# Kernel optimization log

Hardware: AMD Instinct MI355X
Metric: run time of the kernel (lower is better)

Reference implementation:

```python
import jax, jax.numpy as jnp
import numpy as np

IMG_W, IMG_H = 128, 128
N_PTS = 256
MIN_D, MAX_D = 2.0, 6.0
FOCAL = 1.7320508  # 1/tan(fov/2), fov=60deg (FoVPerspectiveCameras default)
SCALING = 0.1      # scaling_factor default
EPS_EA = 1e-10     # pytorch3d EmissionAbsorptionRaymarcher eps


def setup_inputs() -> dict:
    key = jax.random.key(0)
    k1, k2 = jax.random.split(key)
    image3d = jax.random.uniform(k1, (1, 1, 128, 128, 128), jnp.float32)
    opacity = jax.random.uniform(k2, (1, 1, 128, 128, 128), jnp.float32)
    # row-vector camera convention (pytorch3d): p_cam = p_world @ R + T
    R = jnp.zeros((1, 3, 3), jnp.float32).at[:, jnp.arange(3), jnp.arange(3)].set(1.0)
    T = jnp.zeros((1, 3), jnp.float32).at[:, 2].set(4.0)
    return {"image3d": image3d, "opacity": opacity, "R": R, "T": T}


def _trilinear(vol, pts):
    """vol [C,D,H,W]; pts [N,3] xyz in [-1,1] (x->W, y->H, z->D).
    align_corners=True, zero padding outside. Returns [N,C]."""
    C, D, H, W = vol.shape
    x = (pts[:, 0] + 1.0) * 0.5 * (W - 1)
    y = (pts[:, 1] + 1.0) * 0.5 * (H - 1)
    z = (pts[:, 2] + 1.0) * 0.5 * (D - 1)
    x0 = jnp.floor(x); y0 = jnp.floor(y); z0 = jnp.floor(z)
    wx = x - x0; wy = y - y0; wz = z - z0
    vol_flat = vol.reshape(C, -1)
    out = jnp.zeros((pts.shape[0], C), vol.dtype)
    for dz in (0, 1):
        for dy in (0, 1):
            for dx in (0, 1):
                xi = (x0 + dx).astype(jnp.int32)
                yi = (y0 + dy).astype(jnp.int32)
                zi = (z0 + dz).astype(jnp.int32)
                valid = ((xi >= 0) & (xi < W) & (yi >= 0) & (yi < H)
                         & (zi >= 0) & (zi < D))
                w = ((wx if dx else 1.0 - wx) * (wy if dy else 1.0 - wy)
                     * (wz if dz else 1.0 - wz)) * valid.astype(vol.dtype)
                idx = ((jnp.clip(zi, 0, D - 1) * H + jnp.clip(yi, 0, H - 1)) * W
                       + jnp.clip(xi, 0, W - 1))
                vals = jnp.take(vol_flat, idx, axis=1)  # [C,N]
                out = out + w[:, None] * vals.T
    return out


def _forward(image3d, opacity, R, T):
    B = image3d.shape[0]
    features_vol = jnp.repeat(image3d, 3, axis=1)            # [B,3,D,H,W]
    densities_vol = opacity * SCALING                        # [B,1,D,H,W]
    Dv, Hv, Wv = image3d.shape[2:]
    shape = max(image3d.shape[1], image3d.shape[2])
    voxel = 3.0 / shape
    half_extent = voxel * (jnp.array([Wv, Hv, Dv], jnp.float32) - 1.0) / 2.0

    # NDC pixel grid (pytorch3d: +x left, +y up)
    xs = jnp.linspace(1.0, -1.0, IMG_W)
    ys = jnp.linspace(1.0, -1.0, IMG_H)
    gy, gx = jnp.meshgrid(ys, xs, indexing="ij")             # [H,W]
    dirs_cam = jnp.stack([gx / FOCAL, gy / FOCAL, jnp.ones_like(gx)], -1)  # [H,W,3]
    depths = jnp.linspace(MIN_D, MAX_D, N_PTS)               # [P]

    # row-vector transforms: p_world = (p_cam - T) @ R^T
    origins = jnp.einsum("bi,bji->bj", -T, R)                # camera centers [B,3]
    dirs_world = jnp.einsum("hwi,bji->bhwj", dirs_cam, R)    # [B,H,W,3]
    pts = (origins[:, None, None, None, :]
           + depths[None, None, None, :, None] * dirs_world[:, :, :, None, :])
    local = pts / half_extent                                # [B,H,W,P,3]

    pts_flat = local.reshape(B, -1, 3)
    feats = jax.vmap(_trilinear)(features_vol, pts_flat)
    feats = feats.reshape(B, IMG_H, IMG_W, N_PTS, 3)
    dens = jax.vmap(_trilinear)(densities_vol, pts_flat)
    dens = dens.reshape(B, IMG_H, IMG_W, N_PTS)

    # EmissionAbsorption raymarcher
    cum = jnp.cumprod((1.0 + EPS_EA) - dens, axis=-1)
    absorption = jnp.concatenate([jnp.ones_like(cum[..., :1]), cum[..., :-1]], -1)
    weights = dens * absorption
    feat_out = jnp.sum(weights[..., None] * feats, axis=-2)  # [B,H,W,3]
    opac = 1.0 - jnp.prod(1.0 - dens, axis=-1, keepdims=True)
    rgba = jnp.concatenate([feat_out, opac], axis=-1)        # [B,H,W,4]

    screen = jnp.transpose(rgba, (0, 3, 2, 1))               # permute(0,3,2,1)
    gray = screen[:, :3].mean(axis=1, keepdims=True)         # [B,1,W,H]
    st = (gray - gray.mean()) / (gray.std(ddof=1) + 1e-8)    # standardized
    out = (st - st.min() + 1e-8) / (st.max() - st.min() + 1e-8)  # normalized
    return out


def reference(image3d, opacity, R, T):
    return _forward(image3d, opacity, R, T)
```

## Files before the change

### kernel.cpp

```cpp
#include <hip/hip_runtime.h>
#include <math.h>


#define FOCAL 1.7320508f

__global__ __launch_bounds__(256) void render_kernel(
    const float* __restrict__ img, const float* __restrict__ opa,
    const float* __restrict__ Rm, const float* __restrict__ Tv,
    float2* __restrict__ partial, int nseg_shift)
{
  const int lane   = threadIdx.x & 63;
  const int waveid = threadIdx.x >> 6;
  const int wg     = (blockIdx.x << 2) + waveid;
  const int nseg   = 1 << nseg_shift;
  const int seg    = wg & (nseg - 1);
  const int pg     = wg >> nseg_shift;
  const int h      = pg >> 1;
  const int w      = ((pg & 1) << 6) | lane;

  const float R00=Rm[0], R01=Rm[1], R02=Rm[2];
  const float R10=Rm[3], R11=Rm[4], R12=Rm[5];
  const float R20=Rm[6], R21=Rm[7], R22=Rm[8];
  const float T0=Tv[0], T1=Tv[1], T2=Tv[2];

  const float ox = -(T0*R00 + T1*R01 + T2*R02);
  const float oy = -(T0*R10 + T1*R11 + T2*R12);
  const float oz = -(T0*R20 + T1*R21 + T2*R22);

  const float gx = 1.0f - (2.0f/127.0f) * (float)w;
  const float gy = 1.0f - (2.0f/127.0f) * (float)h;
  const float dcx = gx * (1.0f/FOCAL);
  const float dcy = gy * (1.0f/FOCAL);
  const float dwx = dcx*R00 + dcy*R01 + R02;
  const float dwy = dcx*R10 + dcy*R11 + R12;
  const float dwz = dcx*R20 + dcy*R21 + R22;

  const float s_he = (1.0f/1.48828125f) * 63.5f;
  const float ax = dwx * s_he, bx = ox * s_he + 63.5f;
  const float ay = dwy * s_he, by = oy * s_he + 63.5f;
  const float az = dwz * s_he, bz = oz * s_he + 63.5f;

  const int spseg = 256 >> nseg_shift;
  const int p0 = seg * spseg;

  float lp = 1.0f;
  float accl = 0.0f;

  for (int j = 0; j < spseg; ++j) {
    const float depth = 2.0f + (4.0f/255.0f) * (float)(p0 + j);
    const float x = bx + depth * ax;
    const float y = by + depth * ay;
    const float z = bz + depth * az;
    const float x0f = floorf(x), y0f = floorf(y), z0f = floorf(z);
    const float wx = x - x0f, wy = y - y0f, wz = z - z0f;
    const int x0 = (int)x0f, y0 = (int)y0f, z0 = (int)z0f;

    float feat = 0.0f, dens = 0.0f;
    if (x0 >= -1 && x0 <= 127 && y0 >= -1 && y0 <= 127 &&
        z0 >= -1 && z0 <= 127) {
      const float fx0 = (x0 >= 0)   ? (1.0f - wx) : 0.0f;
      const float fx1 = (x0 <= 126) ? wx          : 0.0f;
      const float fy0 = (y0 >= 0)   ? (1.0f - wy) : 0.0f;
      const float fy1 = (y0 <= 126) ? wy          : 0.0f;
      const float fz0 = (z0 >= 0)   ? (1.0f - wz) : 0.0f;
      const float fz1 = (z0 <= 126) ? wz          : 0.0f;
      const int ix0 = (x0 >= 0)   ? x0     : 0;
      const int ix1 = (x0 <= 126) ? x0 + 1 : 127;
      const int iy0 = ((y0 >= 0)   ? y0     : 0)   << 7;
      const int iy1 = ((y0 <= 126) ? y0 + 1 : 127) << 7;
      const int iz0 = ((z0 >= 0)   ? z0     : 0)   << 14;
      const int iz1 = ((z0 <= 126) ? z0 + 1 : 127) << 14;

      const int b00 = iz0 + iy0, b01 = iz0 + iy1;
      const int b10 = iz1 + iy0, b11 = iz1 + iy1;
      const float w00 = fz0*fy0, w01 = fz0*fy1, w10 = fz1*fy0, w11 = fz1*fy1;

      feat = w00*(fx0*img[b00+ix0] + fx1*img[b00+ix1])
           + w01*(fx0*img[b01+ix0] + fx1*img[b01+ix1])
           + w10*(fx0*img[b10+ix0] + fx1*img[b10+ix1])
           + w11*(fx0*img[b11+ix0] + fx1*img[b11+ix1]);
      dens = w00*(fx0*opa[b00+ix0] + fx1*opa[b00+ix1])
           + w01*(fx0*opa[b01+ix0] + fx1*opa[b01+ix1])
           + w10*(fx0*opa[b10+ix0] + fx1*opa[b10+ix1])
           + w11*(fx0*opa[b11+ix0] + fx1*opa[b11+ix1]);
    }
    const float d = dens * 0.1f;
    accl += feat * d * lp;
    lp   *= (1.0f - d);
  }

  partial[(seg << 14) + (h << 7) + w] = make_float2(accl, lp);
}

__global__ __launch_bounds__(256) void combine_kernel(
    const float2* __restrict__ partial, float* __restrict__ g,
    double* __restrict__ bstats, int nseg)
{
  const int tid = threadIdx.x;
  const int pid = (blockIdx.x << 8) + tid;

  float T = 1.0f, acc = 0.0f;
  for (int s = 0; s < nseg; ++s) {
    const float2 v = partial[(s << 14) + pid];
    acc += v.x * T;
    T *= v.y;
  }
  g[pid] = acc;

  double sum = (double)acc;
  double sq  = (double)acc * (double)acc;
  float mn = acc, mx = acc;
  #pragma unroll
  for (int off = 32; off >= 1; off >>= 1) {
    sum += __shfl_xor(sum, off, 64);
    sq  += __shfl_xor(sq,  off, 64);
    mn = fminf(mn, __shfl_xor(mn, off, 64));
    mx = fmaxf(mx, __shfl_xor(mx, off, 64));
  }
  __shared__ double s_sum[4], s_sq[4];
  __shared__ float  s_mn[4], s_mx[4];
  const int wv = tid >> 6;
  if ((tid & 63) == 0) { s_sum[wv]=sum; s_sq[wv]=sq; s_mn[wv]=mn; s_mx[wv]=mx; }
  __syncthreads();
  if (tid == 0) {
    double S = 0.0, Q = 0.0;
    float MN = s_mn[0], MX = s_mx[0];
    #pragma unroll
    for (int i = 0; i < 4; ++i) {
      S += s_sum[i]; Q += s_sq[i];
      MN = fminf(MN, s_mn[i]); MX = fmaxf(MX, s_mx[i]);
    }
    bstats[(blockIdx.x << 2) + 0] = S;
    bstats[(blockIdx.x << 2) + 1] = Q;
    bstats[(blockIdx.x << 2) + 2] = (double)MN;
    bstats[(blockIdx.x << 2) + 3] = (double)MX;
  }
}

__global__ __launch_bounds__(256) void finalize_kernel(
    const float* __restrict__ g, const double* __restrict__ bstats,
    float* __restrict__ out)
{
  __shared__ float sh[3];
  const int tid = threadIdx.x;
  if (tid < 64) {
    double S  = bstats[(tid << 2) + 0];
    double Q  = bstats[(tid << 2) + 1];
    double MN = bstats[(tid << 2) + 2];
    double MX = bstats[(tid << 2) + 3];
    #pragma unroll
    for (int off = 32; off >= 1; off >>= 1) {
      S += __shfl_xor(S, off, 64);
      Q += __shfl_xor(Q, off, 64);
      MN = fmin(MN, __shfl_xor(MN, off, 64));
      MX = fmax(MX, __shfl_xor(MX, off, 64));
    }
    if (tid == 0) {
      const double mean = S / 16384.0;
      double var = (Q - 16384.0 * mean * mean) / 16383.0;
      if (var < 0.0) var = 0.0;
      const float sdev = (float)sqrt(var) + 1e-8f;
      const float mnf = (float)MN, mxf = (float)MX;
      sh[0] = mnf;
      sh[1] = 1.0f / sdev;
      sh[2] = 1.0f / ((mxf - mnf) / sdev + 1e-8f);
    }
  }
  __syncthreads();
  const float mnv = sh[0], invs = sh[1], sc = sh[2];
  const int pid = (blockIdx.x << 8) + tid;
  const float v = g[pid];
  const int hh = pid >> 7, ww = pid & 127;
  out[(ww << 7) + hh] = ((v - mnv) * invs + 1e-8f) * sc;
}

extern "C" void kernel_launch(void* const* d_in, const int* in_sizes, int n_in,
                              void* d_out, int out_size, void* d_ws, size_t ws_size,
                              hipStream_t stream) {
  const float* img = (const float*)d_in[0];
  const float* opa = (const float*)d_in[1];
  const float* Rm  = (const float*)d_in[2];
  const float* Tv  = (const float*)d_in[3];
  float* out = (float*)d_out;

  int shift = 4;
  while (shift > 0) {
    const size_t need = ((size_t)131072 << shift) + 65536 + 2048;
    if (need <= ws_size) break;
    --shift;
  }
  const int nseg = 1 << shift;

  char* wsb = (char*)d_ws;
  float2* partial = (float2*)wsb;
  float*  g       = (float*)(wsb + ((size_t)131072 << shift));
  double* bstats  = (double*)(wsb + ((size_t)131072 << shift) + 65536);

  render_kernel<<<64 * nseg, 256, 0, stream>>>(img, opa, Rm, Tv, partial, shift);
  combine_kernel<<<64, 256, 0, stream>>>(partial, g, bstats, nseg);
  finalize_kernel<<<64, 256, 0, stream>>>(g, bstats, out);
}
```

Measured before the change: 98.67 us.

## Fuse render, segment combine and normalization into one kernel with last-block finalize

Merges the three launches into a single kernel. Each block handles 64 pixels with 8 waves, each wave marching one 32-sample segment, and the segments are combined through shared memory instead of a global partial buffer. Global statistics are reduced by whichever block finishes last, detected with an atomic counter, and that block writes the normalized output. This removes two launches and the partial-buffer round trip, but the ray march runs on 256 blocks instead of up to 1024, the final normalization pass is serialized onto one block, and a memset is added.

```diff
diff --git a/kernel.cpp b/kernel.cpp
--- a/kernel.cpp
+++ b/kernel.cpp
@@ -4,19 +4,18 @@
 
 #define FOCAL 1.7320508f
 
-__global__ __launch_bounds__(256) void render_kernel(
+__global__ __launch_bounds__(512) void dvr_kernel(
     const float* __restrict__ img, const float* __restrict__ opa,
     const float* __restrict__ Rm, const float* __restrict__ Tv,
-    float2* __restrict__ partial, int nseg_shift)
+    float* __restrict__ g, double* __restrict__ bstats,
+    unsigned int* __restrict__ counter, float* __restrict__ out)
 {
-  const int lane   = threadIdx.x & 63;
-  const int waveid = threadIdx.x >> 6;
-  const int wg     = (blockIdx.x << 2) + waveid;
-  const int nseg   = 1 << nseg_shift;
-  const int seg    = wg & (nseg - 1);
-  const int pg     = wg >> nseg_shift;
-  const int h      = pg >> 1;
-  const int w      = ((pg & 1) << 6) | lane;
+  const int tid  = threadIdx.x;
+  const int lane = tid & 63;
+  const int seg  = tid >> 6;
+  const int b    = blockIdx.x;
+  const int h    = b >> 1;
+  const int w    = ((b & 1) << 6) | lane;
 
   const float R00=Rm[0], R01=Rm[1], R02=Rm[2];
   const float R10=Rm[3], R11=Rm[4], R12=Rm[5];
@@ -36,21 +35,20 @@
   const float dwz = dcx*R20 + dcy*R21 + R22;
 
   const float s_he = (1.0f/1.48828125f) * 63.5f;
-  const float ax = dwx * s_he, bx = ox * s_he + 63.5f;
-  const float ay = dwy * s_he, by = oy * s_he + 63.5f;
-  const float az = dwz * s_he, bz = oz * s_he + 63.5f;
+  const float ax = dwx * s_he, bxc = ox * s_he + 63.5f;
+  const float ay = dwy * s_he, byc = oy * s_he + 63.5f;
+  const float az = dwz * s_he, bzc = oz * s_he + 63.5f;
 
-  const int spseg = 256 >> nseg_shift;
-  const int p0 = seg * spseg;
+  const int p0 = seg << 5;
 
   float lp = 1.0f;
   float accl = 0.0f;
 
-  for (int j = 0; j < spseg; ++j) {
+  for (int j = 0; j < 32; ++j) {
     const float depth = 2.0f + (4.0f/255.0f) * (float)(p0 + j);
-    const float x = bx + depth * ax;
-    const float y = by + depth * ay;
-    const float z = bz + depth * az;
+    const float x = bxc + depth * ax;
+    const float y = byc + depth * ay;
+    const float z = bzc + depth * az;
     const float x0f = floorf(x), y0f = floorf(y), z0f = floorf(z);
     const float wx = x - x0f, wy = y - y0f, wz = z - z0f;
     const int x0 = (int)x0f, y0 = (int)y0f, z0 = (int)z0f;
@@ -89,89 +87,93 @@
     lp   *= (1.0f - d);
   }
 
-  partial[(seg << 14) + (h << 7) + w] = make_float2(accl, lp);
-}
+  __shared__ float2 slp[8][64];
+  slp[seg][lane] = make_float2(accl, lp);
+  __syncthreads();
 
-__global__ __launch_bounds__(256) void combine_kernel(
-    const float2* __restrict__ partial, float* __restrict__ g,
-    double* __restrict__ bstats, int nseg)
-{
-  const int tid = threadIdx.x;
-  const int pid = (blockIdx.x << 8) + tid;
+  if (tid < 64) {
+    float T = 1.0f, acc = 0.0f;
+    #pragma unroll
+    for (int s = 0; s < 8; ++s) {
+      const float2 v = slp[s][tid];
+      acc += v.x * T;
+      T *= v.y;
+    }
+    const int ww = ((b & 1) << 6) | tid;
+    g[(ww << 7) + h] = acc;
 
-  float T = 1.0f, acc = 0.0f;
-  for (int s = 0; s < nseg; ++s) {
-    const float2 v = partial[(s << 14) + pid];
-    acc += v.x * T;
-    T *= v.y;
-  }
-  g[pid] = acc;
-
-  double sum = (double)acc;
-  double sq  = (double)acc * (double)acc;
-  float mn = acc, mx = acc;
-  #pragma unroll
-  for (int off = 32; off >= 1; off >>= 1) {
-    sum += __shfl_xor(sum, off, 64);
-    sq  += __shfl_xor(sq,  off, 64);
-    mn = fminf(mn, __shfl_xor(mn, off, 64));
-    mx = fmaxf(mx, __shfl_xor(mx, off, 64));
-  }
-  __shared__ double s_sum[4], s_sq[4];
-  __shared__ float  s_mn[4], s_mx[4];
-  const int wv = tid >> 6;
-  if ((tid & 63) == 0) { s_sum[wv]=sum; s_sq[wv]=sq; s_mn[wv]=mn; s_mx[wv]=mx; }
-  __syncthreads();
-  if (tid == 0) {
-    double S = 0.0, Q = 0.0;
-    float MN = s_mn[0], MX = s_mx[0];
-    #pragma unroll
-    for (int i = 0; i < 4; ++i) {
-      S += s_sum[i]; Q += s_sq[i];
-      MN = fminf(MN, s_mn[i]); MX = fmaxf(MX, s_mx[i]);
-    }
-    bstats[(blockIdx.x << 2) + 0] = S;
-    bstats[(blockIdx.x << 2) + 1] = Q;
-    bstats[(blockIdx.x << 2) + 2] = (double)MN;
-    bstats[(blockIdx.x << 2) + 3] = (double)MX;
-  }
-}
-
-__global__ __launch_bounds__(256) void finalize_kernel(
-    const float* __restrict__ g, const double* __restrict__ bstats,
-    float* __restrict__ out)
-{
-  __shared__ float sh[3];
-  const int tid = threadIdx.x;
-  if (tid < 64) {
-    double S  = bstats[(tid << 2) + 0];
-    double Q  = bstats[(tid << 2) + 1];
-    double MN = bstats[(tid << 2) + 2];
-    double MX = bstats[(tid << 2) + 3];
+    double sum = (double)acc;
+    double sq  = (double)acc * (double)acc;
+    float mn = acc, mx = acc;
     #pragma unroll
     for (int off = 32; off >= 1; off >>= 1) {
-      S += __shfl_xor(S, off, 64);
-      Q += __shfl_xor(Q, off, 64);
-      MN = fmin(MN, __shfl_xor(MN, off, 64));
-      MX = fmax(MX, __shfl_xor(MX, off, 64));
+      sum += __shfl_xor(sum, off, 64);
+      sq  += __shfl_xor(sq,  off, 64);
+      mn = fminf(mn, __shfl_xor(mn, off, 64));
+      mx = fmaxf(mx, __shfl_xor(mx, off, 64));
     }
     if (tid == 0) {
-      const double mean = S / 16384.0;
-      double var = (Q - 16384.0 * mean * mean) / 16383.0;
-      if (var < 0.0) var = 0.0;
-      const float sdev = (float)sqrt(var) + 1e-8f;
-      const float mnf = (float)MN, mxf = (float)MX;
-      sh[0] = mnf;
-      sh[1] = 1.0f / sdev;
-      sh[2] = 1.0f / ((mxf - mnf) / sdev + 1e-8f);
+      bstats[(b << 2) + 0] = sum;
+      bstats[(b << 2) + 1] = sq;
+      bstats[(b << 2) + 2] = (double)mn;
+      bstats[(b << 2) + 3] = (double)mx;
     }
   }
   __syncthreads();
-  const float mnv = sh[0], invs = sh[1], sc = sh[2];
-  const int pid = (blockIdx.x << 8) + tid;
-  const float v = g[pid];
-  const int hh = pid >> 7, ww = pid & 127;
-  out[(ww << 7) + hh] = ((v - mnv) * invs + 1e-8f) * sc;
+
+  __shared__ int is_last;
+  if (tid == 0) {
+    __threadfence();
+    const unsigned int old = atomicAdd(counter, 1u);
+    is_last = (old == gridDim.x - 1) ? 1 : 0;
+  }
+  __syncthreads();
+  if (!is_last) return;
+  __threadfence();
+
+  double S = 0.0, Q = 0.0;
+  float MN = 3.402823466e38f, MX = -3.402823466e38f;
+  if (tid < 256) {
+    S  = bstats[(tid << 2) + 0];
+    Q  = bstats[(tid << 2) + 1];
+    MN = (float)bstats[(tid << 2) + 2];
+    MX = (float)bstats[(tid << 2) + 3];
+  }
+  #pragma unroll
+  for (int off = 32; off >= 1; off >>= 1) {
+    S += __shfl_xor(S, off, 64);
+    Q += __shfl_xor(Q, off, 64);
+    MN = fminf(MN, __shfl_xor(MN, off, 64));
+    MX = fmaxf(MX, __shfl_xor(MX, off, 64));
+  }
+  __shared__ double rs[8], rq[8];
+  __shared__ float rmn[8], rmx[8];
+  if (lane == 0) { rs[seg] = S; rq[seg] = Q; rmn[seg] = MN; rmx[seg] = MX; }
+  __syncthreads();
+
+  __shared__ float cmn, cinvs, csc;
+  if (tid == 0) {
+    double St = 0.0, Qt = 0.0;
+    float MNt = rmn[0], MXt = rmx[0];
+    #pragma unroll
+    for (int i = 0; i < 8; ++i) {
+      St += rs[i]; Qt += rq[i];
+      MNt = fminf(MNt, rmn[i]); MXt = fmaxf(MXt, rmx[i]);
+    }
+    const double mean = St / 16384.0;
+    double var = (Qt - 16384.0 * mean * mean) / 16383.0;
+    if (var < 0.0) var = 0.0;
+    const float sdev = (float)sqrt(var) + 1e-8f;
+    cmn   = MNt;
+    cinvs = 1.0f / sdev;
+    csc   = 1.0f / ((MXt - MNt) / sdev + 1e-8f);
+  }
+  __syncthreads();
+
+  const float mnv = cmn, invs = cinvs, sc = csc;
+  for (int i = tid; i < 16384; i += 512) {
+    out[i] = ((g[i] - mnv) * invs + 1e-8f) * sc;
+  }
 }
 
 extern "C" void kernel_launch(void* const* d_in, const int* in_sizes, int n_in,
@@ -183,20 +185,11 @@
   const float* Tv  = (const float*)d_in[3];
   float* out = (float*)d_out;
 
-  int shift = 4;
-  while (shift > 0) {
-    const size_t need = ((size_t)131072 << shift) + 65536 + 2048;
-    if (need <= ws_size) break;
-    --shift;
-  }
-  const int nseg = 1 << shift;
+  char* wsb = (char*)d_ws;
+  float*        g       = (float*)wsb;
+  double*       bstats  = (double*)(wsb + 65536);
+  unsigned int* counter = (unsigned int*)(wsb + 65536 + 8192);
 
-  char* wsb = (char*)d_ws;
-  float2* partial = (float2*)wsb;
-  float*  g       = (float*)(wsb + ((size_t)131072 << shift));
-  double* bstats  = (double*)(wsb + ((size_t)131072 << shift) + 65536);
-
-  render_kernel<<<64 * nseg, 256, 0, stream>>>(img, opa, Rm, Tv, partial, shift);
-  combine_kernel<<<64, 256, 0, stream>>>(partial, g, bstats, nseg);
-  finalize_kernel<<<64, 256, 0, stream>>>(g, bstats, out);
+  hipMemsetAsync(counter, 0, sizeof(unsigned int), stream);
+  dvr_kernel<<<256, 512, 0, stream>>>(img, opa, Rm, Tv, g, bstats, counter, out);
 }
```

After: 104.1 us. +5.5%, slower.
